# Kernel optimization log

Hardware: AMD Instinct MI355X
Metric: run time of the kernel (lower is better)

Reference implementation:

```python
import jax, jax.numpy as jnp
import numpy as np

N_NODES = 20000
N_EDGES = 320000
N_GRAPHS = 64
SEQ = 20
SCALAR = 16
EMB = 32
HID = 128
HEADS = 4
IN_DIM = SCALAR + 5 * EMB  # 176
NEG_SLOPE = 0.2


def masked_mean_embed(table, idx):
    # table: [V, EMB], idx: [N, L] with 0 = padding
    emb = table[idx]                                  # [N, L, EMB]
    mask = (idx != 0).astype(emb.dtype)[..., None]    # [N, L, 1]
    return (emb * mask).sum(axis=1) / (mask.sum(axis=1) + 1e-9)


def gat_conv(x, src, dst, W, att_src, att_dst, bias, heads, out_ch):
    # PyG GATConv (add_self_loops already applied to src/dst), concat heads.
    N = x.shape[0]
    xw = (x @ W).reshape(N, heads, out_ch)            # [N, H, C]
    a_src = (xw * att_src).sum(-1)                    # [N, H]
    a_dst = (xw * att_dst).sum(-1)                    # [N, H]
    e = jax.nn.leaky_relu(a_src[src] + a_dst[dst], NEG_SLOPE)  # [E, H]
    e_max = jax.ops.segment_max(e, dst, num_segments=N)
    e_max = jnp.where(jnp.isfinite(e_max), e_max, 0.0)
    ex = jnp.exp(e - e_max[dst])                      # [E, H]
    denom = jax.ops.segment_sum(ex, dst, num_segments=N)
    alpha = ex / (denom[dst] + 1e-16)                 # [E, H]
    msg = xw[src] * alpha[:, :, None]                 # [E, H, C]
    out = jax.ops.segment_sum(msg, dst, num_segments=N)
    return out.reshape(N, heads * out_ch) + bias


def setup_inputs() -> dict:
    key = jax.random.key(0)
    ks = jax.random.split(key, 24)
    s = 0.05
    inp = {
        "x_scalar": jax.random.normal(ks[0], (N_NODES, SCALAR), jnp.float32),
        "x_opcode": jax.random.randint(ks[1], (N_NODES, SEQ), 0, 256),
        "x_source": jax.random.randint(ks[2], (N_NODES, SEQ), 0, 512),
        "x_sink": jax.random.randint(ks[3], (N_NODES, SEQ), 0, 512),
        "x_string_manip": jax.random.randint(ks[4], (N_NODES, SEQ), 0, 128),
        "x_payload": jax.random.randint(ks[5], (N_NODES, SEQ), 0, 1024),
        "edge_index": jax.random.randint(ks[6], (2, N_EDGES), 0, N_NODES),
        "batch": jnp.sort(jax.random.randint(ks[7], (N_NODES,), 0, N_GRAPHS)),
        # embedding tables (row 0 = padding; masked out anyway)
        "emb_opcode": jax.random.normal(ks[8], (256, EMB)) * s,
        "emb_source": jax.random.normal(ks[9], (512, EMB)) * s,
        "emb_sink": jax.random.normal(ks[10], (512, EMB)) * s,
        "emb_string": jax.random.normal(ks[11], (128, EMB)) * s,
        "emb_payload": jax.random.normal(ks[12], (1024, EMB)) * s,
        "ln_gamma": jnp.ones((IN_DIM,), jnp.float32),
        "ln_beta": jnp.zeros((IN_DIM,), jnp.float32),
        "W1": jax.random.normal(ks[13], (IN_DIM, HEADS * HID)) * s,
        "att_src1": jax.random.normal(ks[14], (HEADS, HID)) * s,
        "att_dst1": jax.random.normal(ks[15], (HEADS, HID)) * s,
        "b1": jnp.zeros((HEADS * HID,), jnp.float32),
        "W2": jax.random.normal(ks[16], (HEADS * HID, HID)) * s,
        "att_src2": jax.random.normal(ks[17], (1, HID)) * s,
        "att_dst2": jax.random.normal(ks[18], (1, HID)) * s,
        "b2": jnp.zeros((HID,), jnp.float32),
        "cls_w1": jax.random.normal(ks[19], (HID, HID // 2)) * s,
        "cls_b1": jnp.zeros((HID // 2,), jnp.float32),
        "cls_w2": jax.random.normal(ks[20], (HID // 2, 2)) * s,
        "cls_b2": jnp.zeros((2,), jnp.float32),
    }
    return inp


def reference(x_scalar, x_opcode, x_source, x_sink, x_string_manip, x_payload,
              edge_index, batch,
              emb_opcode, emb_source, emb_sink, emb_string, emb_payload,
              ln_gamma, ln_beta,
              W1, att_src1, att_dst1, b1,
              W2, att_src2, att_dst2, b2,
              cls_w1, cls_b1, cls_w2, cls_b2):
    feats = jnp.concatenate([
        x_scalar,
        masked_mean_embed(emb_opcode, x_opcode),
        masked_mean_embed(emb_source, x_source),
        masked_mean_embed(emb_sink, x_sink),
        masked_mean_embed(emb_string, x_string_manip),
        masked_mean_embed(emb_payload, x_payload),
    ], axis=1)  # [N, 176]
    mu = feats.mean(-1, keepdims=True)
    var = ((feats - mu) ** 2).mean(-1, keepdims=True)
    h = (feats - mu) / jnp.sqrt(var + 1e-5) * ln_gamma + ln_beta

    # add self loops (PyG GATConv default)
    loops = jnp.arange(N_NODES, dtype=edge_index.dtype)
    src = jnp.concatenate([edge_index[0], loops])
    dst = jnp.concatenate([edge_index[1], loops])

    x = jax.nn.elu(gat_conv(h, src, dst, W1, att_src1, att_dst1, b1, HEADS, HID))
    x = jax.nn.elu(gat_conv(x, src, dst, W2, att_src2, att_dst2, b2, 1, HID))

    pooled = jax.ops.segment_max(x, batch, num_segments=N_GRAPHS)  # [G, HID]
    hcls = jax.nn.relu(pooled @ cls_w1 + cls_b1)
    return hcls @ cls_w2 + cls_b2  # [G, 2]
```

## Files before the change

### kernel.cpp

```cpp
#include <hip/hip_runtime.h>
#include <hip/hip_bf16.h>
#include <math.h>

#define N_NODES 20000
#define N_EDGES 320000
#define N_GRAPHS 64
#define SEQ 20
#define SCALAR 16
#define EMB 32
#define HID 128
#define IN_DIM 176
#define TOT_EDGES (N_EDGES + N_NODES)
#define CHUNK_SMALL 10000
#define POOL_SLICES 32

typedef _Float16 half8v __attribute__((ext_vector_type(8)));
typedef float f32x4 __attribute__((ext_vector_type(4)));
#define LO_SCALE 2048.0f
#define LO_INV (1.0f / 2048.0f)

#define PB2_ELEMS (16 * 8 * 64 * 8)
#define PB1_ELEMS (4 * 6 * 8 * 64 * 8)

#define SETUP_BLOCKS 124
#define COUNT_BLOCKS ((TOT_EDGES + 255) / 256)
#define NB4 ((N_NODES + 3) / 4)

__device__ inline float readlane_f(float v, int l) {
  return __uint_as_float(__builtin_amdgcn_readlane(__float_as_uint(v), l));
}
__device__ inline int readlane_i(int v, int l) {
  return __builtin_amdgcn_readlane(v, l);
}
__device__ inline float leaky(float e) { return e >= 0.f ? e : 0.2f * e; }
__device__ inline float elu(float v) { return v > 0.f ? v : expf(v) - 1.f; }

__global__ __launch_bounds__(256) void setup_count_kernel(
    const float* __restrict__ W1, const float* __restrict__ att_s1,
    const float* __restrict__ att_d1, const float* __restrict__ W2,
    const int* __restrict__ edge_index, const int* __restrict__ batch,
    float* __restrict__ was4, float* __restrict__ wad4,
    _Float16* __restrict__ PB1h, _Float16* __restrict__ PB1l,
    _Float16* __restrict__ PB2h, _Float16* __restrict__ PB2l,
    int* __restrict__ cnt, int* __restrict__ gstarts) {
  int b = blockIdx.x;
  if (b < 44) {
    int lane = threadIdx.x & 63;
    int k = b * 4 + (threadIdx.x >> 6);
    if (k >= IN_DIM) return;
    const float* wrow = W1 + (size_t)k * 512;
    float s[4], d[4];
#pragma unroll
    for (int hh = 0; hh < 4; ++hh) {
      float w0 = wrow[hh * 128 + lane], w1 = wrow[hh * 128 + 64 + lane];
      float a0 = att_s1[hh * 128 + lane], a1 = att_s1[hh * 128 + 64 + lane];
      float c0 = att_d1[hh * 128 + lane], c1 = att_d1[hh * 128 + 64 + lane];
      s[hh] = w0 * a0 + w1 * a1;
      d[hh] = w0 * c0 + w1 * c1;
    }
    for (int off = 1; off < 64; off <<= 1) {
#pragma unroll
      for (int hh = 0; hh < 4; ++hh) {
        s[hh] += __shfl_xor(s[hh], off);
        d[hh] += __shfl_xor(d[hh], off);
      }
    }
    if (lane == 0) {
      *(float4*)&was4[k * 4] = make_float4(s[0], s[1], s[2], s[3]);
      *(float4*)&wad4[k * 4] = make_float4(d[0], d[1], d[2], d[3]);
    }
  } else if (b < 92) {
    int t = (b - 44) * 256 + threadIdx.x;
    int lane = t & 63, wi = t >> 6;
    int r = lane & 15, g = lane >> 4;
    int ntile = wi & 7, rem = wi >> 3;
    int ks = rem % 6, hh = rem / 6;
    int col = hh * 128 + ntile * 16 + r;
    size_t o = ((size_t)wi * 64 + lane) * 8;
#pragma unroll
    for (int j = 0; j < 8; ++j) {
      int k = ks * 32 + g * 8 + j;
      float v = (k < IN_DIM) ? W1[(size_t)k * 512 + col] : 0.f;
      _Float16 h = (_Float16)v;
      PB1h[o + j] = h;
      PB1l[o + j] = (_Float16)((v - (float)h) * LO_SCALE);
    }
  } else if (b < SETUP_BLOCKS) {
    int t = (b - 92) * 256 + threadIdx.x;
    int lane = t & 63, wi = t >> 6;
    int r = lane & 15, g = lane >> 4;
    int ks = wi >> 3, ntile = wi & 7;
    int col = ntile * 16 + r;
    size_t o = ((size_t)wi * 64 + lane) * 8;
#pragma unroll
    for (int j = 0; j < 8; ++j) {
      int k = ks * 32 + g * 8 + j;
      float v = W2[(size_t)k * 128 + col];
      _Float16 h = (_Float16)v;
      PB2h[o + j] = h;
      PB2l[o + j] = (_Float16)((v - (float)h) * LO_SCALE);
    }
  } else if (b < SETUP_BLOCKS + COUNT_BLOCKS) {
    int i = (b - SETUP_BLOCKS) * 256 + threadIdx.x;
    if (i < N_EDGES) {
      atomicAdd(&cnt[edge_index[N_EDGES + i]], 1);
    } else if (i < TOT_EDGES) {
      atomicAdd(&cnt[i - N_EDGES], 1);
    }
  } else {
    int t = threadIdx.x;
    if (t > N_GRAPHS) return;
    int lo = 0, hi = N_NODES;
    while (lo < hi) {
      int mid = (lo + hi) >> 1;
      if (batch[mid] < t) lo = mid + 1; else hi = mid;
    }
    gstarts[t] = lo;
  }
}

__global__ __launch_bounds__(1024) void prefix_kernel(const int* __restrict__ cnt,
                                                      int* __restrict__ indptr,
                                                      int n, int total) {
  __shared__ int ss[1024];
  int t = threadIdx.x;
  int per = (n + 1023) / 1024;
  int beg = t * per, end = min(beg + per, n);
  int s = 0;
  for (int i = beg; i < end; ++i) s += cnt[i];
  ss[t] = s;
  __syncthreads();
  for (int off = 1; off < 1024; off <<= 1) {
    int v = (t >= off) ? ss[t - off] : 0;
    __syncthreads();
    ss[t] += v;
    __syncthreads();
  }
  int run = ss[t] - s;
  for (int i = beg; i < end; ++i) { indptr[i] = run; run += cnt[i]; }
  if (t == 0) indptr[n] = total;
}

__global__ __launch_bounds__(256) void feats_scatter_kernel(
    const int* __restrict__ edge_index, const int* __restrict__ indptr,
    int* __restrict__ cursor, int* __restrict__ srcs,
    const float* __restrict__ xs,
    const int* __restrict__ i0, const int* __restrict__ i1,
    const int* __restrict__ i2, const int* __restrict__ i3,
    const int* __restrict__ i4,
    const float* __restrict__ t0, const float* __restrict__ t1,
    const float* __restrict__ t2, const float* __restrict__ t3,
    const float* __restrict__ t4,
    const float* __restrict__ gamma, const float* __restrict__ beta,
    const float* __restrict__ was4, const float* __restrict__ wad4,
    float* __restrict__ hout, float* __restrict__ a_s,
    float* __restrict__ a_d) {
  int b = blockIdx.x;
  if (b >= NB4) {
    int i = (b - NB4) * 256 + threadIdx.x;
    int s, d;
    if (i < N_EDGES) { s = edge_index[i]; d = edge_index[N_EDGES + i]; }
    else if (i < TOT_EDGES) { s = i - N_EDGES; d = s; }
    else return;
    int pos = indptr[d] + atomicAdd(&cursor[d], 1);
    srcs[pos] = s;
    return;
  }
  int lane = threadIdx.x & 63;
  int w = threadIdx.x >> 6;
  int n = b * 4 + w;
  if (n >= N_NODES) return;
  __shared__ int sidx[4][100];
  {
    int j = lane;
    int tab = j / 20, l = j - tab * 20;
    const int* ip = tab == 0 ? i0 : tab == 1 ? i1 : tab == 2 ? i2 : i3;
    sidx[w][j] = ip[n * SEQ + l];
    if (lane < 36) {
      int j2 = 64 + lane;
      int tab2 = j2 / 20, l2 = j2 - tab2 * 20;
      const int* ip2 = tab2 == 3 ? i3 : i4;
      sidx[w][j2] = ip2[n * SEQ + l2];
    }
  }
  bool l48 = lane < 48;
  float f0, f1, f2 = 0.f;
  if (lane < SCALAR) {
    f0 = xs[n * SCALAR + lane];
  } else {
    int tt = lane - SCALAR, tab = tt >> 5, d = tt & 31;
    const float* tp = tab == 0 ? t0 : t1;
    float sum = 0.f, cnt = 0.f;
#pragma unroll
    for (int l = 0; l < SEQ; ++l) {
      int id = sidx[w][tab * 20 + l];
      if (id != 0) { sum += tp[id * EMB + d]; cnt += 1.f; }
    }
    f0 = sum / (cnt + 1e-9f);
  }
  {
    int tt = 48 + lane, tab = tt >> 5, d = tt & 31;
    const float* tp = tab == 1 ? t1 : tab == 2 ? t2 : t3;
    float sum = 0.f, cnt = 0.f;
#pragma unroll
    for (int l = 0; l < SEQ; ++l) {
      int id = sidx[w][tab * 20 + l];
      if (id != 0) { sum += tp[id * EMB + d]; cnt += 1.f; }
    }
    f1 = sum / (cnt + 1e-9f);
  }
  if (l48) {
    int tt = 112 + lane, tab = tt >> 5, d = tt & 31;
    const float* tp = tab == 3 ? t3 : t4;
    float sum = 0.f, cnt = 0.f;
#pragma unroll
    for (int l = 0; l < SEQ; ++l) {
      int id = sidx[w][tab * 20 + l];
      if (id != 0) { sum += tp[id * EMB + d]; cnt += 1.f; }
    }
    f2 = sum / (cnt + 1e-9f);
  }
  float s = f0 + f1 + f2;
  for (int off = 1; off < 64; off <<= 1) s += __shfl_xor(s, off);
  float mu = s / (float)IN_DIM;
  float v = (f0 - mu) * (f0 - mu) + (f1 - mu) * (f1 - mu) +
            (l48 ? (f2 - mu) * (f2 - mu) : 0.f);
  for (int off = 1; off < 64; off <<= 1) v += __shfl_xor(v, off);
  float rstd = 1.0f / sqrtf(v / (float)IN_DIM + 1e-5f);
  float hv0 = (f0 - mu) * rstd * gamma[lane] + beta[lane];
  float hv1 = (f1 - mu) * rstd * gamma[64 + lane] + beta[64 + lane];
  float hv2 = l48 ? (f2 - mu) * rstd * gamma[128 + lane] + beta[128 + lane] : 0.f;
  float* hr = hout + (size_t)n * IN_DIM;
  hr[lane] = hv0;
  hr[64 + lane] = hv1;
  if (l48) hr[128 + lane] = hv2;

  const float4* wsv = (const float4*)was4;
  const float4* wdv = (const float4*)wad4;
  float4 wsa = wsv[lane], wsb = wsv[64 + lane];
  float4 wsc = l48 ? wsv[128 + lane] : make_float4(0.f, 0.f, 0.f, 0.f);
  float4 wda = wdv[lane], wdb = wdv[64 + lane];
  float4 wdc = l48 ? wdv[128 + lane] : make_float4(0.f, 0.f, 0.f, 0.f);
  float ps0 = hv0 * wsa.x + hv1 * wsb.x + hv2 * wsc.x;
  float ps1 = hv0 * wsa.y + hv1 * wsb.y + hv2 * wsc.y;
  float ps2 = hv0 * wsa.z + hv1 * wsb.z + hv2 * wsc.z;
  float ps3 = hv0 * wsa.w + hv1 * wsb.w + hv2 * wsc.w;
  float pd0 = hv0 * wda.x + hv1 * wdb.x + hv2 * wdc.x;
  float pd1 = hv0 * wda.y + hv1 * wdb.y + hv2 * wdc.y;
  float pd2 = hv0 * wda.z + hv1 * wdb.z + hv2 * wdc.z;
  float pd3 = hv0 * wda.w + hv1 * wdb.w + hv2 * wdc.w;
  for (int off = 1; off < 64; off <<= 1) {
    ps0 += __shfl_xor(ps0, off); ps1 += __shfl_xor(ps1, off);
    ps2 += __shfl_xor(ps2, off); ps3 += __shfl_xor(ps3, off);
    pd0 += __shfl_xor(pd0, off); pd1 += __shfl_xor(pd1, off);
    pd2 += __shfl_xor(pd2, off); pd3 += __shfl_xor(pd3, off);
  }
  if (lane == 0) {
    *(float4*)&a_s[n * 4] = make_float4(ps0, ps1, ps2, ps3);
    *(float4*)&a_d[n * 4] = make_float4(pd0, pd1, pd2, pd3);
  }
}

__global__ __launch_bounds__(256) void agg1h_kernel(
    const float* __restrict__ h, const float* __restrict__ a_src,
    const float* __restrict__ a_dst, const int* __restrict__ indptr,
    const int* __restrict__ srcs, _Float16* __restrict__ agghh,
    _Float16* __restrict__ agghl, int n0, int nM) {
  int lane = threadIdx.x & 63;
  int ln = blockIdx.x * 4 + (threadIdx.x >> 6);
  if (ln >= nM) return;
  int n = n0 + ln;
  int beg = indptr[n], end = indptr[n + 1];
  int deg = end - beg;
  float4 ad = *(const float4*)&a_dst[n * 4];
  bool l48 = lane < 48;
  float acc[4][3] = {};

  auto body = [&](int s, float al0, float al1, float al2, float al3) {
    const float* r = h + (size_t)s * IN_DIM;
    float v0 = r[lane];
    float v1 = r[64 + lane];
    float v2 = l48 ? r[128 + lane] : 0.f;
    acc[0][0] += al0 * v0; acc[0][1] += al0 * v1; acc[0][2] += al0 * v2;
    acc[1][0] += al1 * v0; acc[1][1] += al1 * v1; acc[1][2] += al1 * v2;
    acc[2][0] += al2 * v0; acc[2][1] += al2 * v1; acc[2][2] += al2 * v2;
    acc[3][0] += al3 * v0; acc[3][1] += al3 * v1; acc[3][2] += al3 * v2;
  };

  if (deg <= 64) {
    int j = beg + lane;
    int s = 0;
    float e0 = -INFINITY, e1 = -INFINITY, e2 = -INFINITY, e3 = -INFINITY;
    if (j < end) {
      s = srcs[j];
      float4 as = *(const float4*)&a_src[s * 4];
      e0 = leaky(as.x + ad.x); e1 = leaky(as.y + ad.y);
      e2 = leaky(as.z + ad.z); e3 = leaky(as.w + ad.w);
    }
    float m0 = e0, m1 = e1, m2 = e2, m3 = e3;
    for (int off = 1; off < 64; off <<= 1) {
      m0 = fmaxf(m0, __shfl_xor(m0, off)); m1 = fmaxf(m1, __shfl_xor(m1, off));
      m2 = fmaxf(m2, __shfl_xor(m2, off)); m3 = fmaxf(m3, __shfl_xor(m3, off));
    }
    float x0 = (j < end) ? expf(e0 - m0) : 0.f;
    float x1 = (j < end) ? expf(e1 - m1) : 0.f;
    float x2 = (j < end) ? expf(e2 - m2) : 0.f;
    float x3 = (j < end) ? expf(e3 - m3) : 0.f;
    float d0 = x0, d1 = x1, d2 = x2, d3 = x3;
    for (int off = 1; off < 64; off <<= 1) {
      d0 += __shfl_xor(d0, off); d1 += __shfl_xor(d1, off);
      d2 += __shfl_xor(d2, off); d3 += __shfl_xor(d3, off);
    }
    float al0 = x0 / (d0 + 1e-16f), al1 = x1 / (d1 + 1e-16f);
    float al2 = x2 / (d2 + 1e-16f), al3 = x3 / (d3 + 1e-16f);
    int jj = 0;
    for (; jj + 2 <= deg; jj += 2) {
      int sa = readlane_i(s, jj), sb = readlane_i(s, jj + 1);
      float a0 = readlane_f(al0, jj), a1 = readlane_f(al1, jj);
      float a2 = readlane_f(al2, jj), a3 = readlane_f(al3, jj);
      float b0 = readlane_f(al0, jj + 1), b1 = readlane_f(al1, jj + 1);
      float b2 = readlane_f(al2, jj + 1), b3 = readlane_f(al3, jj + 1);
      body(sa, a0, a1, a2, a3);
      body(sb, b0, b1, b2, b3);
    }
    if (jj < deg) {
      int sa = readlane_i(s, jj);
      body(sa, readlane_f(al0, jj), readlane_f(al1, jj),
           readlane_f(al2, jj), readlane_f(al3, jj));
    }
  } else {
    float m0 = -INFINITY, m1 = -INFINITY, m2 = -INFINITY, m3 = -INFINITY;
    for (int j0 = beg; j0 < end; j0 += 64) {
      int j = j0 + lane;
      if (j < end) {
        int s = srcs[j];
        float4 as = *(const float4*)&a_src[s * 4];
        m0 = fmaxf(m0, leaky(as.x + ad.x)); m1 = fmaxf(m1, leaky(as.y + ad.y));
        m2 = fmaxf(m2, leaky(as.z + ad.z)); m3 = fmaxf(m3, leaky(as.w + ad.w));
      }
    }
    for (int off = 1; off < 64; off <<= 1) {
      m0 = fmaxf(m0, __shfl_xor(m0, off)); m1 = fmaxf(m1, __shfl_xor(m1, off));
      m2 = fmaxf(m2, __shfl_xor(m2, off)); m3 = fmaxf(m3, __shfl_xor(m3, off));
    }
    float d0 = 0.f, d1 = 0.f, d2 = 0.f, d3 = 0.f;
    for (int j0 = beg; j0 < end; j0 += 64) {
      int j = j0 + lane;
      if (j < end) {
        int s = srcs[j];
        float4 as = *(const float4*)&a_src[s * 4];
        d0 += expf(leaky(as.x + ad.x) - m0); d1 += expf(leaky(as.y + ad.y) - m1);
        d2 += expf(leaky(as.z + ad.z) - m2); d3 += expf(leaky(as.w + ad.w) - m3);
      }
    }
    for (int off = 1; off < 64; off <<= 1) {
      d0 += __shfl_xor(d0, off); d1 += __shfl_xor(d1, off);
      d2 += __shfl_xor(d2, off); d3 += __shfl_xor(d3, off);
    }
    float r0 = 1.f / (d0 + 1e-16f), r1 = 1.f / (d1 + 1e-16f);
    float r2 = 1.f / (d2 + 1e-16f), r3 = 1.f / (d3 + 1e-16f);
    for (int j0 = beg; j0 < end; j0 += 64) {
      int jn = min(64, end - j0);
      int j = j0 + lane;
      int s = 0;
      float al0 = 0.f, al1 = 0.f, al2 = 0.f, al3 = 0.f;
      if (j < end) {
        s = srcs[j];
        float4 as = *(const float4*)&a_src[s * 4];
        al0 = expf(leaky(as.x + ad.x) - m0) * r0;
        al1 = expf(leaky(as.y + ad.y) - m1) * r1;
        al2 = expf(leaky(as.z + ad.z) - m2) * r2;
        al3 = expf(leaky(as.w + ad.w) - m3) * r3;
      }
      for (int jj = 0; jj < jn; ++jj) {
        body(readlane_i(s, jj), readlane_f(al0, jj), readlane_f(al1, jj),
             readlane_f(al2, jj), readlane_f(al3, jj));
      }
    }
  }

  size_t base = (size_t)ln * (4 * IN_DIM);
#pragma unroll
  for (int hh = 0; hh < 4; ++hh) {
    size_t o0 = base + hh * IN_DIM + lane;
    float v0 = acc[hh][0], v1 = acc[hh][1];
    _Float16 h0 = (_Float16)v0, h1 = (_Float16)v1;
    agghh[o0] = h0;      agghl[o0] = (_Float16)((v0 - (float)h0) * LO_SCALE);
    agghh[o0 + 64] = h1; agghl[o0 + 64] = (_Float16)((v1 - (float)h1) * LO_SCALE);
    if (l48) {
      float v2 = acc[hh][2];
      _Float16 h2 = (_Float16)v2;
      agghh[o0 + 128] = h2;
      agghl[o0 + 128] = (_Float16)((v2 - (float)h2) * LO_SCALE);
    }
  }
}

__global__ __launch_bounds__(512) void gemm_fused_kernel(
    const _Float16* __restrict__ Ah, const _Float16* __restrict__ Al,
    const half8v* __restrict__ PB1h, const half8v* __restrict__ PB1l,
    const float* __restrict__ b1,
    const half8v* __restrict__ PB2h, const half8v* __restrict__ PB2l,
    const float* __restrict__ att_s, const float* __restrict__ att_d,
    float* __restrict__ xw2, float* __restrict__ a_s, float* __restrict__ a_d,
    int n0, int nM) {
  __shared__ _Float16 s1h[32][520];
  __shared__ _Float16 s1l[32][520];
  int lane = threadIdx.x & 63;
  int w = threadIdx.x >> 6;
  int rows0 = blockIdx.x * 32;
  if (rows0 >= nM) return;
  int r = lane & 15, g = lane >> 4;
  int r1 = (rows0 + 16 + r < nM) ? (rows0 + 16 + r) : (rows0 + r);

  {
    int hh = w >> 1, colhalf = w & 1;
    f32x4 acc[2][4] = {};
    f32x4 accm[2][4] = {};
    const _Float16* a0h = Ah + ((size_t)(rows0 + r) * 4 + hh) * IN_DIM;
    const _Float16* a0l = Al + ((size_t)(rows0 + r) * 4 + hh) * IN_DIM;
    const _Float16* a1h = Ah + ((size_t)r1 * 4 + hh) * IN_DIM;
    const _Float16* a1l = Al + ((size_t)r1 * 4 + hh) * IN_DIM;
#pragma unroll 2
    for (int ks = 0; ks < 6; ++ks) {
      int kg = ks * 32 + g * 8;
      int koff = (kg + 8 <= IN_DIM) ? kg : 0;
      half8v ah0 = *(const half8v*)(a0h + koff);
      half8v al0 = *(const half8v*)(a0l + koff);
      half8v ah1 = *(const half8v*)(a1h + koff);
      half8v al1 = *(const half8v*)(a1l + koff);
      const half8v* bh = PB1h + (size_t)(((hh * 6 + ks) * 8 + colhalf * 4) * 64) + lane;
      const half8v* bl = PB1l + (size_t)(((hh * 6 + ks) * 8 + colhalf * 4) * 64) + lane;
#pragma unroll
      for (int nt = 0; nt < 4; ++nt) {
        half8v bhv = bh[nt * 64], blv = bl[nt * 64];
        accm[0][nt] = __builtin_amdgcn_mfma_f32_16x16x32_f16(al0, bhv, accm[0][nt], 0, 0, 0);
        accm[0][nt] = __builtin_amdgcn_mfma_f32_16x16x32_f16(ah0, blv, accm[0][nt], 0, 0, 0);
        acc[0][nt]  = __builtin_amdgcn_mfma_f32_16x16x32_f16(ah0, bhv, acc[0][nt], 0, 0, 0);
        accm[1][nt] = __builtin_amdgcn_mfma_f32_16x16x32_f16(al1, bhv, accm[1][nt], 0, 0, 0);
        accm[1][nt] = __builtin_amdgcn_mfma_f32_16x16x32_f16(ah1, blv, accm[1][nt], 0, 0, 0);
        acc[1][nt]  = __builtin_amdgcn_mfma_f32_16x16x32_f16(ah1, bhv, acc[1][nt], 0, 0, 0);
      }
    }
#pragma unroll
    for (int nt = 0; nt < 4; ++nt) {
      int col = hh * 128 + colhalf * 64 + nt * 16 + r;
      float bb = b1[col];
#pragma unroll
      for (int mt = 0; mt < 2; ++mt) {
#pragma unroll
        for (int i = 0; i < 4; ++i) {
          int row = mt * 16 + g * 4 + i;
          if (rows0 + row < nM) {
            float o = elu(acc[mt][nt][i] + accm[mt][nt][i] * LO_INV + bb);
            _Float16 oh = (_Float16)o;
            s1h[row][col] = oh;
            s1l[row][col] = (_Float16)((o - (float)oh) * LO_SCALE);
          }
        }
      }
    }
  }
  __syncthreads();

  {
    f32x4 qacc[2] = {};
    f32x4 qaccm[2] = {};
#pragma unroll 2
    for (int ks = 0; ks < 16; ++ks) {
      half8v ah0 = *(const half8v*)&s1h[r][ks * 32 + g * 8];
      half8v al0 = *(const half8v*)&s1l[r][ks * 32 + g * 8];
      half8v ah1 = *(const half8v*)&s1h[16 + r][ks * 32 + g * 8];
      half8v al1 = *(const half8v*)&s1l[16 + r][ks * 32 + g * 8];
      half8v bhv = PB2h[(size_t)((ks * 8 + w) * 64) + lane];
      half8v blv = PB2l[(size_t)((ks * 8 + w) * 64) + lane];
      qaccm[0] = __builtin_amdgcn_mfma_f32_16x16x32_f16(al0, bhv, qaccm[0], 0, 0, 0);
      qaccm[0] = __builtin_amdgcn_mfma_f32_16x16x32_f16(ah0, blv, qaccm[0], 0, 0, 0);
      qacc[0]  = __builtin_amdgcn_mfma_f32_16x16x32_f16(ah0, bhv, qacc[0], 0, 0, 0);
      qaccm[1] = __builtin_amdgcn_mfma_f32_16x16x32_f16(al1, bhv, qaccm[1], 0, 0, 0);
      qaccm[1] = __builtin_amdgcn_mfma_f32_16x16x32_f16(ah1, blv, qaccm[1], 0, 0, 0);
      qacc[1]  = __builtin_amdgcn_mfma_f32_16x16x32_f16(ah1, bhv, qacc[1], 0, 0, 0);
    }
    int col = w * 16 + r;
    float as_ = att_s[col], ad_ = att_d[col];
    float ps[2][4], pd[2][4];
#pragma unroll
    for (int mt = 0; mt < 2; ++mt) {
#pragma unroll
      for (int i = 0; i < 4; ++i) {
        float v = qacc[mt][i] + qaccm[mt][i] * LO_INV;
        int row = rows0 + mt * 16 + g * 4 + i;
        if (row < nM) xw2[(size_t)(n0 + row) * 128 + col] = v;
        ps[mt][i] = v * as_;
        pd[mt][i] = v * ad_;
      }
    }
#pragma unroll
    for (int mt = 0; mt < 2; ++mt) {
#pragma unroll
      for (int i = 0; i < 4; ++i) {
        for (int off = 1; off < 16; off <<= 1) {
          ps[mt][i] += __shfl_xor(ps[mt][i], off);
          pd[mt][i] += __shfl_xor(pd[mt][i], off);
        }
      }
    }
    if (r == 0) {
#pragma unroll
      for (int mt = 0; mt < 2; ++mt) {
#pragma unroll
        for (int i = 0; i < 4; ++i) {
          int row = rows0 + mt * 16 + g * 4 + i;
          if (row < nM) {
            atomicAdd(&a_s[n0 + row], ps[mt][i]);
            atomicAdd(&a_d[n0 + row], pd[mt][i]);
          }
        }
      }
    }
  }
}

__global__ __launch_bounds__(256) void agg2_kernel(
    const float* __restrict__ xw, const float* __restrict__ a_src,
    const float* __restrict__ a_dst, const int* __restrict__ indptr,
    const int* __restrict__ srcs, const float* __restrict__ bias,
    float* __restrict__ out) {
  int lane = threadIdx.x & 63;
  int n = blockIdx.x * 4 + (threadIdx.x >> 6);
  if (n >= N_NODES) return;
  int beg = indptr[n], end = indptr[n + 1];
  int deg = end - beg;
  float adn = a_dst[n];
  int half = lane >> 5, l32 = lane & 31;
  float4 acc = make_float4(0.f, 0.f, 0.f, 0.f);

  auto pairs = [&](int s, float al, int jn) {
    int jj = 0;
    for (; jj + 2 <= jn; jj += 2) {
      int sa = readlane_i(s, jj), sb = readlane_i(s, jj + 1);
      float aa = readlane_f(al, jj), ab = readlane_f(al, jj + 1);
      int sh = half ? sb : sa;
      float ahx = half ? ab : aa;
      float4 v = *(const float4*)&xw[(size_t)sh * HID + l32 * 4];
      acc.x += ahx * v.x; acc.y += ahx * v.y; acc.z += ahx * v.z; acc.w += ahx * v.w;
    }
    if (jj < jn) {
      int sa = readlane_i(s, jj);
      float ahx = half ? 0.f : readlane_f(al, jj);
      float4 v = *(const float4*)&xw[(size_t)sa * HID + l32 * 4];
      acc.x += ahx * v.x; acc.y += ahx * v.y; acc.z += ahx * v.z; acc.w += ahx * v.w;
    }
  };

  if (deg <= 64) {
    int j = beg + lane;
    int s = 0;
    float e = -INFINITY;
    if (j < end) { s = srcs[j]; e = leaky(a_src[s] + adn); }
    float m = e;
    for (int off = 1; off < 64; off <<= 1) m = fmaxf(m, __shfl_xor(m, off));
    float x = (j < end) ? expf(e - m) : 0.f;
    float d = x;
    for (int off = 1; off < 64; off <<= 1) d += __shfl_xor(d, off);
    float al = x / (d + 1e-16f);
    pairs(s, al, deg);
  } else {
    float m = -INFINITY;
    for (int j0 = beg; j0 < end; j0 += 64) {
      int j = j0 + lane;
      if (j < end) m = fmaxf(m, leaky(a_src[srcs[j]] + adn));
    }
    for (int off = 1; off < 64; off <<= 1) m = fmaxf(m, __shfl_xor(m, off));
    float d = 0.f;
    for (int j0 = beg; j0 < end; j0 += 64) {
      int j = j0 + lane;
      if (j < end) d += expf(leaky(a_src[srcs[j]] + adn) - m);
    }
    for (int off = 1; off < 64; off <<= 1) d += __shfl_xor(d, off);
    float rd = 1.f / (d + 1e-16f);
    for (int j0 = beg; j0 < end; j0 += 64) {
      int jn = min(64, end - j0);
      int j = j0 + lane;
      int s = 0;
      float al = 0.f;
      if (j < end) {
        s = srcs[j];
        al = expf(leaky(a_src[s] + adn) - m) * rd;
      }
      pairs(s, al, jn);
    }
  }

  acc.x += __shfl_xor(acc.x, 32); acc.y += __shfl_xor(acc.y, 32);
  acc.z += __shfl_xor(acc.z, 32); acc.w += __shfl_xor(acc.w, 32);
  if (half == 0) {
    float4 b = *(const float4*)&bias[l32 * 4];
    float4 o;
    o.x = elu(acc.x + b.x); o.y = elu(acc.y + b.y);
    o.z = elu(acc.z + b.z); o.w = elu(acc.w + b.w);
    *(float4*)&out[(size_t)n * HID + l32 * 4] = o;
  }
}

__global__ __launch_bounds__(HID) void pool_part_kernel(
    const float* __restrict__ out2, const int* __restrict__ gstarts,
    float* __restrict__ part) {
  int g = blockIdx.x, s = blockIdx.y, t = threadIdx.x;
  int beg = gstarts[g], end = gstarts[g + 1];
  int len = end - beg;
  int b0 = beg + (int)(((long long)len * s) / POOL_SLICES);
  int b1 = beg + (int)(((long long)len * (s + 1)) / POOL_SLICES);
  float m = -INFINITY;
  for (int n = b0; n < b1; ++n) m = fmaxf(m, out2[(size_t)n * HID + t]);
  part[((size_t)g * POOL_SLICES + s) * HID + t] = m;
}

__global__ __launch_bounds__(HID) void pool_reduce_kernel(
    const float* __restrict__ part, float* __restrict__ pooled) {
  int g = blockIdx.x, t = threadIdx.x;
  float m = -INFINITY;
#pragma unroll
  for (int s = 0; s < POOL_SLICES; ++s)
    m = fmaxf(m, part[((size_t)g * POOL_SLICES + s) * HID + t]);
  pooled[g * HID + t] = m;
}

__global__ __launch_bounds__(HID) void cls_kernel(const float* __restrict__ pooled,
                                                  const float* __restrict__ w1,
                                                  const float* __restrict__ b1,
                                                  const float* __restrict__ w2,
                                                  const float* __restrict__ b2,
                                                  float* __restrict__ out) {
  int g = blockIdx.x, t = threadIdx.x;
  __shared__ float sp[HID], sh1[HID / 2];
  sp[t] = pooled[g * HID + t];
  __syncthreads();
  if (t < HID / 2) {
    float s = b1[t];
    for (int k = 0; k < HID; ++k) s += sp[k] * w1[k * (HID / 2) + t];
    sh1[t] = fmaxf(s, 0.f);
  }
  __syncthreads();
  if (t < 2) {
    float o = b2[t];
    for (int k = 0; k < HID / 2; ++k) o += sh1[k] * w2[k * 2 + t];
    out[g * 2 + t] = o;
  }
}

extern "C" void kernel_launch(void* const* d_in, const int* in_sizes, int n_in,
                              void* d_out, int out_size, void* d_ws, size_t ws_size,
                              hipStream_t stream) {
  const float* x_scalar = (const float*)d_in[0];
  const int* x_opcode   = (const int*)d_in[1];
  const int* x_source   = (const int*)d_in[2];
  const int* x_sink     = (const int*)d_in[3];
  const int* x_string   = (const int*)d_in[4];
  const int* x_payload  = (const int*)d_in[5];
  const int* edge_index = (const int*)d_in[6];
  const int* batch      = (const int*)d_in[7];
  const float* emb_opcode = (const float*)d_in[8];
  const float* emb_source = (const float*)d_in[9];
  const float* emb_sink   = (const float*)d_in[10];
  const float* emb_string = (const float*)d_in[11];
  const float* emb_payload= (const float*)d_in[12];
  const float* ln_gamma = (const float*)d_in[13];
  const float* ln_beta  = (const float*)d_in[14];
  const float* W1       = (const float*)d_in[15];
  const float* att_src1 = (const float*)d_in[16];
  const float* att_dst1 = (const float*)d_in[17];
  const float* b1       = (const float*)d_in[18];
  const float* W2       = (const float*)d_in[19];
  const float* att_src2 = (const float*)d_in[20];
  const float* att_dst2 = (const float*)d_in[21];
  const float* b2       = (const float*)d_in[22];
  const float* cls_w1   = (const float*)d_in[23];
  const float* cls_b1   = (const float*)d_in[24];
  const float* cls_w2   = (const float*)d_in[25];
  const float* cls_b2   = (const float*)d_in[26];

  auto total_bytes = [&](int chunk) -> size_t {
    size_t f = (size_t)N_NODES * IN_DIM + (size_t)N_NODES * HID * 2 +
               N_NODES * 4 * 2 + N_NODES * 2 + IN_DIM * 4 * 2 + N_GRAPHS * HID;
    size_t ii = (N_NODES + 1) + N_NODES * 2 + TOT_EDGES + (N_GRAPHS + 1);
    size_t f16b = ((size_t)2 * (PB2_ELEMS + PB1_ELEMS) +
                   (size_t)chunk * 4 * IN_DIM * 2) * sizeof(_Float16) + 64;
    size_t poolb = (size_t)N_GRAPHS * POOL_SLICES * HID * 4 + 32;
    return f * 4 + ii * 4 + f16b + poolb + 256;
  };
  int chunk = (ws_size >= total_bytes(N_NODES)) ? N_NODES : CHUNK_SMALL;

  float* h      = (float*)d_ws;
  _Float16* agghh = (_Float16*)(h + (size_t)N_NODES * IN_DIM);
  _Float16* agghl = agghh + (size_t)chunk * 4 * IN_DIM;
  float* xw2    = (float*)(agghl + (size_t)chunk * 4 * IN_DIM);
  float* out2   = xw2 + (size_t)N_NODES * HID;
  float* a1s    = out2 + (size_t)N_NODES * HID;
  float* a1d    = a1s + N_NODES * 4;
  float* was4   = a1d + N_NODES * 4;
  float* wad4   = was4 + IN_DIM * 4;
  float* pooled = wad4 + IN_DIM * 4;
  int* indptr = (int*)(pooled + N_GRAPHS * HID);
  int* cnt    = indptr + (N_NODES + 1);
  int* cursor = cnt + N_NODES;
  float* a2s  = (float*)(cursor + N_NODES);
  float* a2d  = a2s + N_NODES;
  int* srcs   = (int*)(a2d + N_NODES);
  int* gstarts= srcs + TOT_EDGES;
  uintptr_t pal = ((uintptr_t)(gstarts + N_GRAPHS + 1) + 15) & ~(uintptr_t)15;
  _Float16* PB2h = (_Float16*)pal;
  _Float16* PB2l = PB2h + PB2_ELEMS;
  _Float16* PB1h = PB2l + PB2_ELEMS;
  _Float16* PB1l = PB1h + PB1_ELEMS;
  uintptr_t ppal = ((uintptr_t)(PB1l + PB1_ELEMS) + 15) & ~(uintptr_t)15;
  float* pool_part = (float*)ppal;

  hipMemsetAsync(cnt, 0, 4 * N_NODES * sizeof(int), stream);

  setup_count_kernel<<<SETUP_BLOCKS + COUNT_BLOCKS + 1, 256, 0, stream>>>(
      W1, att_src1, att_dst1, W2, edge_index, batch,
      was4, wad4, PB1h, PB1l, PB2h, PB2l, cnt, gstarts);

  prefix_kernel<<<1, 1024, 0, stream>>>(cnt, indptr, N_NODES, TOT_EDGES);

  feats_scatter_kernel<<<NB4 + COUNT_BLOCKS, 256, 0, stream>>>(
      edge_index, indptr, cursor, srcs,
      x_scalar, x_opcode, x_source, x_sink, x_string, x_payload,
      emb_opcode, emb_source, emb_sink, emb_string, emb_payload,
      ln_gamma, ln_beta, was4, wad4, h, a1s, a1d);

  for (int n0 = 0; n0 < N_NODES; n0 += chunk) {
    int nM = min(chunk, N_NODES - n0);
    agg1h_kernel<<<(nM + 3) / 4, 256, 0, stream>>>(h, a1s, a1d, indptr, srcs,
                                                   agghh, agghl, n0, nM);
    gemm_fused_kernel<<<(nM + 31) / 32, 512, 0, stream>>>(
        agghh, agghl, (const half8v*)PB1h, (const half8v*)PB1l, b1,
        (const half8v*)PB2h, (const half8v*)PB2l, att_src2, att_dst2,
        xw2, a2s, a2d, n0, nM);
  }

  agg2_kernel<<<NB4, 256, 0, stream>>>(xw2, a2s, a2d, indptr, srcs, b2, out2);

  pool_part_kernel<<<dim3(N_GRAPHS, POOL_SLICES), HID, 0, stream>>>(out2, gstarts, pool_part);
  pool_reduce_kernel<<<N_GRAPHS, HID, 0, stream>>>(pool_part, pooled);
  cls_kernel<<<N_GRAPHS, HID, 0, stream>>>(pooled, cls_w1, cls_b1, cls_w2, cls_b2, (float*)d_out);
}
```

Before: 353.9 us.

## Regroup setup stages so feature embedding overlaps edge counting and weight packing

The setup work is redistributed across kernels. A small kernel computes the W1·att projections first. The feature/LayerNorm kernel then also does the weight packing, the degree counting atomics and the graph-start search in extra blocks, so the heavy feature gather runs alongside the counting. The prefix scan and the CSR scatter follow as separate kernels. Launch count rises from three to four, trading the extra launch for less serialized work before the prefix scan.

```diff
diff --git a/kernel.cpp b/kernel.cpp
--- a/kernel.cpp
+++ b/kernel.cpp
@@ -22,9 +22,12 @@
 #define PB2_ELEMS (16 * 8 * 64 * 8)
 #define PB1_ELEMS (4 * 6 * 8 * 64 * 8)
 
-#define SETUP_BLOCKS 124
 #define COUNT_BLOCKS ((TOT_EDGES + 255) / 256)
 #define NB4 ((N_NODES + 3) / 4)
+#define L1_PACK1 NB4
+#define L1_PACK2 (NB4 + 48)
+#define L1_COUNT (NB4 + 80)
+#define L1_TOTAL (NB4 + 80 + COUNT_BLOCKS + 1)
 
 __device__ inline float readlane_f(float v, int l) {
   return __uint_as_float(__builtin_amdgcn_readlane(__float_as_uint(v), l));
@@ -35,115 +38,37 @@
 __device__ inline float leaky(float e) { return e >= 0.f ? e : 0.2f * e; }
 __device__ inline float elu(float v) { return v > 0.f ? v : expf(v) - 1.f; }
 
-__global__ __launch_bounds__(256) void setup_count_kernel(
+__global__ __launch_bounds__(256) void wasd_kernel(
     const float* __restrict__ W1, const float* __restrict__ att_s1,
-    const float* __restrict__ att_d1, const float* __restrict__ W2,
-    const int* __restrict__ edge_index, const int* __restrict__ batch,
-    float* __restrict__ was4, float* __restrict__ wad4,
-    _Float16* __restrict__ PB1h, _Float16* __restrict__ PB1l,
-    _Float16* __restrict__ PB2h, _Float16* __restrict__ PB2l,
-    int* __restrict__ cnt, int* __restrict__ gstarts) {
-  int b = blockIdx.x;
-  if (b < 44) {
-    int lane = threadIdx.x & 63;
-    int k = b * 4 + (threadIdx.x >> 6);
-    if (k >= IN_DIM) return;
-    const float* wrow = W1 + (size_t)k * 512;
-    float s[4], d[4];
+    const float* __restrict__ att_d1, float* __restrict__ was4,
+    float* __restrict__ wad4) {
+  int lane = threadIdx.x & 63;
+  int k = blockIdx.x * 4 + (threadIdx.x >> 6);
+  if (k >= IN_DIM) return;
+  const float* wrow = W1 + (size_t)k * 512;
+  float s[4], d[4];
+#pragma unroll
+  for (int hh = 0; hh < 4; ++hh) {
+    float w0 = wrow[hh * 128 + lane], w1 = wrow[hh * 128 + 64 + lane];
+    float a0 = att_s1[hh * 128 + lane], a1 = att_s1[hh * 128 + 64 + lane];
+    float c0 = att_d1[hh * 128 + lane], c1 = att_d1[hh * 128 + 64 + lane];
+    s[hh] = w0 * a0 + w1 * a1;
+    d[hh] = w0 * c0 + w1 * c1;
+  }
+  for (int off = 1; off < 64; off <<= 1) {
 #pragma unroll
     for (int hh = 0; hh < 4; ++hh) {
-      float w0 = wrow[hh * 128 + lane], w1 = wrow[hh * 128 + 64 + lane];
-      float a0 = att_s1[hh * 128 + lane], a1 = att_s1[hh * 128 + 64 + lane];
-      float c0 = att_d1[hh * 128 + lane], c1 = att_d1[hh * 128 + 64 + lane];
-      s[hh] = w0 * a0 + w1 * a1;
-      d[hh] = w0 * c0 + w1 * c1;
-    }
-    for (int off = 1; off < 64; off <<= 1) {
-#pragma unroll
-      for (int hh = 0; hh < 4; ++hh) {
-        s[hh] += __shfl_xor(s[hh], off);
-        d[hh] += __shfl_xor(d[hh], off);
-      }
-    }
-    if (lane == 0) {
-      *(float4*)&was4[k * 4] = make_float4(s[0], s[1], s[2], s[3]);
-      *(float4*)&wad4[k * 4] = make_float4(d[0], d[1], d[2], d[3]);
-    }
-  } else if (b < 92) {
-    int t = (b - 44) * 256 + threadIdx.x;
-    int lane = t & 63, wi = t >> 6;
-    int r = lane & 15, g = lane >> 4;
-    int ntile = wi & 7, rem = wi >> 3;
-    int ks = rem % 6, hh = rem / 6;
-    int col = hh * 128 + ntile * 16 + r;
-    size_t o = ((size_t)wi * 64 + lane) * 8;
-#pragma unroll
-    for (int j = 0; j < 8; ++j) {
-      int k = ks * 32 + g * 8 + j;
-      float v = (k < IN_DIM) ? W1[(size_t)k * 512 + col] : 0.f;
-      _Float16 h = (_Float16)v;
-      PB1h[o + j] = h;
-      PB1l[o + j] = (_Float16)((v - (float)h) * LO_SCALE);
-    }
-  } else if (b < SETUP_BLOCKS) {
-    int t = (b - 92) * 256 + threadIdx.x;
-    int lane = t & 63, wi = t >> 6;
-    int r = lane & 15, g = lane >> 4;
-    int ks = wi >> 3, ntile = wi & 7;
-    int col = ntile * 16 + r;
-    size_t o = ((size_t)wi * 64 + lane) * 8;
-#pragma unroll
-    for (int j = 0; j < 8; ++j) {
-      int k = ks * 32 + g * 8 + j;
-      float v = W2[(size_t)k * 128 + col];
-      _Float16 h = (_Float16)v;
-      PB2h[o + j] = h;
-      PB2l[o + j] = (_Float16)((v - (float)h) * LO_SCALE);
-    }
-  } else if (b < SETUP_BLOCKS + COUNT_BLOCKS) {
-    int i = (b - SETUP_BLOCKS) * 256 + threadIdx.x;
-    if (i < N_EDGES) {
-      atomicAdd(&cnt[edge_index[N_EDGES + i]], 1);
-    } else if (i < TOT_EDGES) {
-      atomicAdd(&cnt[i - N_EDGES], 1);
-    }
-  } else {
-    int t = threadIdx.x;
-    if (t > N_GRAPHS) return;
-    int lo = 0, hi = N_NODES;
-    while (lo < hi) {
-      int mid = (lo + hi) >> 1;
-      if (batch[mid] < t) lo = mid + 1; else hi = mid;
-    }
-    gstarts[t] = lo;
-  }
-}
-
-__global__ __launch_bounds__(1024) void prefix_kernel(const int* __restrict__ cnt,
-                                                      int* __restrict__ indptr,
-                                                      int n, int total) {
-  __shared__ int ss[1024];
-  int t = threadIdx.x;
-  int per = (n + 1023) / 1024;
-  int beg = t * per, end = min(beg + per, n);
-  int s = 0;
-  for (int i = beg; i < end; ++i) s += cnt[i];
-  ss[t] = s;
-  __syncthreads();
-  for (int off = 1; off < 1024; off <<= 1) {
-    int v = (t >= off) ? ss[t - off] : 0;
-    __syncthreads();
-    ss[t] += v;
-    __syncthreads();
-  }
-  int run = ss[t] - s;
-  for (int i = beg; i < end; ++i) { indptr[i] = run; run += cnt[i]; }
-  if (t == 0) indptr[n] = total;
-}
-
-__global__ __launch_bounds__(256) void feats_scatter_kernel(
-    const int* __restrict__ edge_index, const int* __restrict__ indptr,
-    int* __restrict__ cursor, int* __restrict__ srcs,
+      s[hh] += __shfl_xor(s[hh], off);
+      d[hh] += __shfl_xor(d[hh], off);
+    }
+  }
+  if (lane == 0) {
+    *(float4*)&was4[k * 4] = make_float4(s[0], s[1], s[2], s[3]);
+    *(float4*)&wad4[k * 4] = make_float4(d[0], d[1], d[2], d[3]);
+  }
+}
+
+__global__ __launch_bounds__(256) void feats_setup_kernel(
     const float* __restrict__ xs,
     const int* __restrict__ i0, const int* __restrict__ i1,
     const int* __restrict__ i2, const int* __restrict__ i3,
@@ -153,17 +78,63 @@
     const float* __restrict__ t4,
     const float* __restrict__ gamma, const float* __restrict__ beta,
     const float* __restrict__ was4, const float* __restrict__ wad4,
+    const float* __restrict__ W1, const float* __restrict__ W2,
+    const int* __restrict__ edge_index, const int* __restrict__ batch,
     float* __restrict__ hout, float* __restrict__ a_s,
-    float* __restrict__ a_d) {
+    float* __restrict__ a_d,
+    _Float16* __restrict__ PB1h, _Float16* __restrict__ PB1l,
+    _Float16* __restrict__ PB2h, _Float16* __restrict__ PB2l,
+    int* __restrict__ cnt, int* __restrict__ gstarts) {
   int b = blockIdx.x;
   if (b >= NB4) {
-    int i = (b - NB4) * 256 + threadIdx.x;
-    int s, d;
-    if (i < N_EDGES) { s = edge_index[i]; d = edge_index[N_EDGES + i]; }
-    else if (i < TOT_EDGES) { s = i - N_EDGES; d = s; }
-    else return;
-    int pos = indptr[d] + atomicAdd(&cursor[d], 1);
-    srcs[pos] = s;
+    if (b < L1_PACK2) {
+      int t = (b - L1_PACK1) * 256 + threadIdx.x;
+      int lane = t & 63, wi = t >> 6;
+      int r = lane & 15, g = lane >> 4;
+      int ntile = wi & 7, rem = wi >> 3;
+      int ks = rem % 6, hh = rem / 6;
+      int col = hh * 128 + ntile * 16 + r;
+      size_t o = ((size_t)wi * 64 + lane) * 8;
+#pragma unroll
+      for (int j = 0; j < 8; ++j) {
+        int k = ks * 32 + g * 8 + j;
+        float v = (k < IN_DIM) ? W1[(size_t)k * 512 + col] : 0.f;
+        _Float16 h = (_Float16)v;
+        PB1h[o + j] = h;
+        PB1l[o + j] = (_Float16)((v - (float)h) * LO_SCALE);
+      }
+    } else if (b < L1_COUNT) {
+      int t = (b - L1_PACK2) * 256 + threadIdx.x;
+      int lane = t & 63, wi = t >> 6;
+      int r = lane & 15, g = lane >> 4;
+      int ks = wi >> 3, ntile = wi & 7;
+      int col = ntile * 16 + r;
+      size_t o = ((size_t)wi * 64 + lane) * 8;
+#pragma unroll
+      for (int j = 0; j < 8; ++j) {
+        int k = ks * 32 + g * 8 + j;
+        float v = W2[(size_t)k * 128 + col];
+        _Float16 h = (_Float16)v;
+        PB2h[o + j] = h;
+        PB2l[o + j] = (_Float16)((v - (float)h) * LO_SCALE);
+      }
+    } else if (b < L1_COUNT + COUNT_BLOCKS) {
+      int i = (b - L1_COUNT) * 256 + threadIdx.x;
+      if (i < N_EDGES) {
+        atomicAdd(&cnt[edge_index[N_EDGES + i]], 1);
+      } else if (i < TOT_EDGES) {
+        atomicAdd(&cnt[i - N_EDGES], 1);
+      }
+    } else {
+      int t = threadIdx.x;
+      if (t > N_GRAPHS) return;
+      int lo = 0, hi = N_NODES;
+      while (lo < hi) {
+        int mid = (lo + hi) >> 1;
+        if (batch[mid] < t) lo = mid + 1; else hi = mid;
+      }
+      gstarts[t] = lo;
+    }
     return;
   }
   int lane = threadIdx.x & 63;
@@ -190,35 +161,35 @@
   } else {
     int tt = lane - SCALAR, tab = tt >> 5, d = tt & 31;
     const float* tp = tab == 0 ? t0 : t1;
-    float sum = 0.f, cnt = 0.f;
+    float sum = 0.f, cnt2 = 0.f;
 #pragma unroll
     for (int l = 0; l < SEQ; ++l) {
       int id = sidx[w][tab * 20 + l];
-      if (id != 0) { sum += tp[id * EMB + d]; cnt += 1.f; }
-    }
-    f0 = sum / (cnt + 1e-9f);
+      if (id != 0) { sum += tp[id * EMB + d]; cnt2 += 1.f; }
+    }
+    f0 = sum / (cnt2 + 1e-9f);
   }
   {
     int tt = 48 + lane, tab = tt >> 5, d = tt & 31;
     const float* tp = tab == 1 ? t1 : tab == 2 ? t2 : t3;
-    float sum = 0.f, cnt = 0.f;
+    float sum = 0.f, cnt2 = 0.f;
 #pragma unroll
     for (int l = 0; l < SEQ; ++l) {
       int id = sidx[w][tab * 20 + l];
-      if (id != 0) { sum += tp[id * EMB + d]; cnt += 1.f; }
-    }
-    f1 = sum / (cnt + 1e-9f);
+      if (id != 0) { sum += tp[id * EMB + d]; cnt2 += 1.f; }
+    }
+    f1 = sum / (cnt2 + 1e-9f);
   }
   if (l48) {
     int tt = 112 + lane, tab = tt >> 5, d = tt & 31;
     const float* tp = tab == 3 ? t3 : t4;
-    float sum = 0.f, cnt = 0.f;
+    float sum = 0.f, cnt2 = 0.f;
 #pragma unroll
     for (int l = 0; l < SEQ; ++l) {
       int id = sidx[w][tab * 20 + l];
-      if (id != 0) { sum += tp[id * EMB + d]; cnt += 1.f; }
-    }
-    f2 = sum / (cnt + 1e-9f);
+      if (id != 0) { sum += tp[id * EMB + d]; cnt2 += 1.f; }
+    }
+    f2 = sum / (cnt2 + 1e-9f);
   }
   float s = f0 + f1 + f2;
   for (int off = 1; off < 64; off <<= 1) s += __shfl_xor(s, off);
@@ -259,6 +230,41 @@
     *(float4*)&a_s[n * 4] = make_float4(ps0, ps1, ps2, ps3);
     *(float4*)&a_d[n * 4] = make_float4(pd0, pd1, pd2, pd3);
   }
+}
+
+__global__ __launch_bounds__(1024) void prefix_kernel(const int* __restrict__ cnt,
+                                                      int* __restrict__ indptr,
+                                                      int n, int total) {
+  __shared__ int ss[1024];
+  int t = threadIdx.x;
+  int per = (n + 1023) / 1024;
+  int beg = t * per, end = min(beg + per, n);
+  int s = 0;
+  for (int i = beg; i < end; ++i) s += cnt[i];
+  ss[t] = s;
+  __syncthreads();
+  for (int off = 1; off < 1024; off <<= 1) {
+    int v = (t >= off) ? ss[t - off] : 0;
+    __syncthreads();
+    ss[t] += v;
+    __syncthreads();
+  }
+  int run = ss[t] - s;
+  for (int i = beg; i < end; ++i) { indptr[i] = run; run += cnt[i]; }
+  if (t == 0) indptr[n] = total;
+}
+
+__global__ void scatter_kernel(const int* __restrict__ edge_index,
+                               const int* __restrict__ indptr,
+                               int* __restrict__ cursor,
+                               int* __restrict__ srcs) {
+  int i = blockIdx.x * 256 + threadIdx.x;
+  int s, d;
+  if (i < N_EDGES) { s = edge_index[i]; d = edge_index[N_EDGES + i]; }
+  else if (i < TOT_EDGES) { s = i - N_EDGES; d = s; }
+  else return;
+  int pos = indptr[d] + atomicAdd(&cursor[d], 1);
+  srcs[pos] = s;
 }
 
 __global__ __launch_bounds__(256) void agg1h_kernel(
@@ -718,17 +724,19 @@
 
   hipMemsetAsync(cnt, 0, 4 * N_NODES * sizeof(int), stream);
 
-  setup_count_kernel<<<SETUP_BLOCKS + COUNT_BLOCKS + 1, 256, 0, stream>>>(
-      W1, att_src1, att_dst1, W2, edge_index, batch,
-      was4, wad4, PB1h, PB1l, PB2h, PB2l, cnt, gstarts);
-
-  prefix_kernel<<<1, 1024, 0, stream>>>(cnt, indptr, N_NODES, TOT_EDGES);
-
-  feats_scatter_kernel<<<NB4 + COUNT_BLOCKS, 256, 0, stream>>>(
-      edge_index, indptr, cursor, srcs,
+  wasd_kernel<<<(IN_DIM + 3) / 4, 256, 0, stream>>>(W1, att_src1, att_dst1,
+                                                    was4, wad4);
+
+  feats_setup_kernel<<<L1_TOTAL, 256, 0, stream>>>(
       x_scalar, x_opcode, x_source, x_sink, x_string, x_payload,
       emb_opcode, emb_source, emb_sink, emb_string, emb_payload,
-      ln_gamma, ln_beta, was4, wad4, h, a1s, a1d);
+      ln_gamma, ln_beta, was4, wad4, W1, W2, edge_index, batch,
+      h, a1s, a1d, PB1h, PB1l, PB2h, PB2l, cnt, gstarts);
+
+  prefix_kernel<<<1, 1024, 0, stream>>>(cnt, indptr, N_NODES, TOT_EDGES);
+
+  scatter_kernel<<<COUNT_BLOCKS, 256, 0, stream>>>(edge_index, indptr, cursor,
+                                                   srcs);
 
   for (int n0 = 0; n0 < N_NODES; n0 += chunk) {
     int nM = min(chunk, N_NODES - n0);
```

Result: no change. 351.8 us (-0.6%).
